# Kernel optimization log

Hardware: AMD Instinct MI355X
Metric: run time of the kernel (lower is better)

## Reference

```python
import jax, jax.numpy as jnp
import numpy as np
from functools import partial

T, B, CH, H, W = 16, 4, 128, 128, 128
TAU, VTH, ALPHA, EPS = 2.0, 1.0, 2.0, 1e-5

# ATan surrogate-gradient spike (spikingjelly surrogate.ATan, alpha=2.0)
@jax.custom_vjp
def spike(x):
    return (x >= 0.0).astype(x.dtype)

def _spike_fwd(x):
    return spike(x), x

def _spike_bwd(x, g):
    return (g * (ALPHA / 2.0) / (1.0 + (jnp.pi / 2.0 * ALPHA * x) ** 2),)

spike.defvjp(_spike_fwd, _spike_bwd)

def _conv(x, w):  # x [N,C,H,W], w [O,I,3,3], padding=1 -> SAME
    return jax.lax.conv_general_dilated(x, w, (1, 1), 'SAME',
                                        dimension_numbers=('NCHW', 'OIHW', 'NCHW'))

def _bn(x, g, b, m, v):  # inference-mode BatchNorm2d, channel axis 1
    inv = g / jnp.sqrt(v + EPS)
    return x * inv[:, None, None] + (b - m * inv)[:, None, None]

def _pool(x):  # MaxPool2d(2,2), NCHW
    return jax.lax.reduce_window(x, -jnp.inf, jax.lax.max,
                                 (1, 1, 2, 2), (1, 1, 2, 2), 'VALID')

def _lif(xs):  # xs [T, ...]; LIFNode: tau=2, v_th=1, v_reset=0, decay_input, hard reset (detached)
    def step(v, x):
        v = v + (x - v) / TAU                      # charge
        s = spike(v - VTH)                         # fire (Heaviside fwd, ATan bwd)
        v = v * (1.0 - jax.lax.stop_gradient(s))   # detached hard reset to 0
        return v, s
    return jax.lax.scan(step, jnp.zeros_like(xs[0]), xs)[1]

def _block(xs, w, g, b, m, v):  # conv -> BN -> LIF -> maxpool, xs [T,B,C,H,W]
    t, bs = xs.shape[0], xs.shape[1]
    y = _bn(_conv(xs.reshape((t * bs,) + xs.shape[2:]), w), g, b, m, v)
    y = _lif(y.reshape((t, bs) + y.shape[1:]))
    y = _pool(y.reshape((t * bs,) + y.shape[2:]))
    return y.reshape((t, bs) + y.shape[1:])


def setup_inputs() -> dict:
    key = jax.random.key(0)
    ks = jax.random.split(key, 8)
    inp = {'x': jax.random.uniform(ks[0], (T, B, 2, H, W), jnp.float32)}
    fan_ins = [2 * 9, CH * 9, CH * 9, CH * 9]
    for i in range(4):
        cin = 2 if i == 0 else CH
        inp[f'w{i+1}'] = jax.random.normal(ks[i + 1], (CH, cin, 3, 3), jnp.float32) * np.sqrt(2.0 / fan_ins[i]).astype(np.float32)
        inp[f'g{i+1}'] = jnp.ones((CH,), jnp.float32)
        inp[f'b{i+1}'] = jnp.zeros((CH,), jnp.float32)
        inp[f'm{i+1}'] = jnp.zeros((CH,), jnp.float32)
        inp[f'v{i+1}'] = jnp.ones((CH,), jnp.float32)
    inp['wfc'] = jax.random.normal(ks[5], (10, CH * 8 * 8), jnp.float32) * np.sqrt(1.0 / (CH * 64)).astype(np.float32)
    inp['bfc'] = jnp.zeros((10,), jnp.float32)
    return inp


def reference(x, w1, g1, b1, m1, v1, w2, g2, b2, m2, v2,
              w3, g3, b3, m3, v3, w4, g4, b4, m4, v4, wfc, bfc):
    y = _block(x, w1, g1, b1, m1, v1)   # [T,B,CH,64,64]
    y = _block(y, w2, g2, b2, m2, v2)   # [T,B,CH,32,32]
    y = _block(y, w3, g3, b3, m3, v3)   # [T,B,CH,16,16]
    y = _block(y, w4, g4, b4, m4, v4)   # [T,B,CH,8,8]
    z = y.reshape(y.shape[0], y.shape[1], -1) @ wfc.T + bfc  # [T,B,10]
    return _lif(z)                       # output spike train [T,B,10]
```

## Files before the change

### kernel.cpp

```cpp
#include <hip/hip_runtime.h>
#include <hip/hip_bf16.h>
#include <math.h>

#define T_STEPS 16

typedef __attribute__((ext_vector_type(8))) short bf16x8;
typedef __attribute__((ext_vector_type(16))) float f32x16;

__global__ __launch_bounds__(256) void prep_w_kernel(const float* __restrict__ w,
                                                     __hip_bfloat16* __restrict__ wp) {
  int idx = blockIdx.x * 256 + threadIdx.x;
  if (idx >= 147456) return;
  int co = idx / 1152, rem = idx - co * 1152;
  int ci = rem / 9, tap = rem - ci * 9;
  float x = w[idx];
  float h = (float)__float2bfloat16(x);
  float r1 = x - h;
  float m = (float)__float2bfloat16(r1);
  float r2 = r1 - m;
  size_t base = (((size_t)tap * 16 + (ci >> 3)) * 128 + co) * 8 + (ci & 7);
  const size_t SSZ = 147456;
  wp[base] = __float2bfloat16(h);
  wp[SSZ + base] = __float2bfloat16(m);
  wp[2 * SSZ + base] = __float2bfloat16(r2);
}

__global__ __launch_bounds__(192) void pad_x_kernel(const float* __restrict__ x,
                                                    float* __restrict__ xp) {
  const int plane = blockIdx.x;
  const int row = blockIdx.y;
  const int c = threadIdx.x;
  if (c < 132) {
    float v = 0.f;
    int gr = row - 1, gc = c - 1;
    if ((unsigned)gr < 128u && (unsigned)gc < 128u)
      v = x[(size_t)plane * 16384 + gr * 128 + gc];
    xp[((size_t)plane * 130 + row) * 132 + c] = v;
  }
}

__global__ __launch_bounds__(256) void layer1_kernel(
    const float* __restrict__ xp, const float* __restrict__ w,
    const float* __restrict__ gn, const float* __restrict__ bn,
    const float* __restrict__ mn, const float* __restrict__ vn,
    __hip_bfloat16* __restrict__ out) {
  const int tid = threadIdx.x;
  const int tile = blockIdx.x;
  const int ty0 = (tile >> 2) * 32, tx0 = (tile & 3) * 32;
  const int co0 = blockIdx.y * 4;
  const int b = blockIdx.z;
  const int qx2 = (tid & 15) * 2;
  const int qy2 = (tid >> 4) * 2;
  const int yq = ty0 + qy2;
  const int xq = tx0 + qx2;

  float wreg[2][9][4];
#pragma unroll
  for (int j = 0; j < 4; ++j)
#pragma unroll
    for (int ci = 0; ci < 2; ++ci)
#pragma unroll
      for (int tap = 0; tap < 9; ++tap)
        wreg[ci][tap][j] = w[(co0 + j) * 18 + ci * 9 + tap];

  float scale[4], shift[4];
#pragma unroll
  for (int j = 0; j < 4; ++j) {
    float inv = gn[co0 + j] / sqrtf(vn[co0 + j] + 1e-5f);
    scale[j] = inv;
    shift[j] = bn[co0 + j] - mn[co0 + j] * inv;
  }

  float vm[4][4];
#pragma unroll
  for (int j = 0; j < 4; ++j)
#pragma unroll
    for (int p = 0; p < 4; ++p) vm[j][p] = 0.f;

  for (int t = 0; t < T_STEPS; ++t) {
    const float* xpt = xp + (size_t)((t * 4 + b) * 2) * 17160;
    float iv[2][4][4];
#pragma unroll
    for (int ci = 0; ci < 2; ++ci)
#pragma unroll
      for (int r = 0; r < 4; ++r)
        *(float4*)&iv[ci][r][0] =
            *(const float4*)(xpt + (size_t)(ci * 130 + yq + r) * 132 + xq);

    float acc[4][4];
#pragma unroll
    for (int j = 0; j < 4; ++j)
#pragma unroll
      for (int p = 0; p < 4; ++p) acc[j][p] = 0.f;

#pragma unroll
    for (int ci = 0; ci < 2; ++ci)
#pragma unroll
      for (int tap = 0; tap < 9; ++tap) {
        const int dy = tap / 3, dx = tap - dy * 3;
#pragma unroll
        for (int sy = 0; sy < 2; ++sy)
#pragma unroll
          for (int sx = 0; sx < 2; ++sx) {
            float xin = iv[ci][sy + dy][sx + dx];
            acc[0][sy * 2 + sx] += wreg[ci][tap][0] * xin;
            acc[1][sy * 2 + sx] += wreg[ci][tap][1] * xin;
            acc[2][sy * 2 + sx] += wreg[ci][tap][2] * xin;
            acc[3][sy * 2 + sx] += wreg[ci][tap][3] * xin;
          }
      }

    const int py = (ty0 >> 1) + (tid >> 4);
    const int px = (tx0 >> 1) + (tid & 15);
    short4 pk;
    short* pks = (short*)&pk;
#pragma unroll
    for (int j = 0; j < 4; ++j) {
      float mx = -1e30f;
#pragma unroll
      for (int p = 0; p < 4; ++p) {
        float yv = acc[j][p] * scale[j] + shift[j];
        float nv = vm[j][p] + (yv - vm[j][p]) * 0.5f;
        mx = fmaxf(mx, nv);
        vm[j][p] = (nv >= 1.0f) ? 0.f : nv;
      }
      __hip_bfloat16 bv = __float2bfloat16(mx >= 1.0f ? 1.0f : 0.0f);
      pks[j] = *(short*)&bv;
    }
    *(short4*)(out + (((size_t)(t * 4 + b) * 64 + py) * 64 + px) * 128 + co0) = pk;
  }
}

template <int S>
__global__ __launch_bounds__(256) void conv32_kernel(
    const __hip_bfloat16* __restrict__ spk, const __hip_bfloat16* __restrict__ wp,
    float* __restrict__ pre, int t_base) {
  constexpr int TILES_X = S / 8;
  const int tile = blockIdx.x;
  const int ty0 = (tile / TILES_X) * 16;
  const int tx0 = (tile % TILES_X) * 8;
  const int tbl = blockIdx.z;
  const int tbg = t_base * 4 + tbl;
  const int tid = threadIdx.x;
  const int lane = tid & 63;
  const int wv = tid >> 6;

  __shared__ uint4 At4[2880];

  const __hip_bfloat16* sp = spk + (size_t)tbg * S * S * 128;
#pragma unroll
  for (int k = 0; k < 12; ++k) {
    int job = k * 256 + tid;
    if (job < 2880) {
      int c8 = job & 15, r = job >> 4;
      int y = (r * 6554) >> 16;
      int xx = r - y * 10;
      int gy = ty0 - 1 + y, gx = tx0 - 1 + xx;
      uint4 v = make_uint4(0u, 0u, 0u, 0u);
      if ((unsigned)gy < (unsigned)S && (unsigned)gx < (unsigned)S)
        v = *(const uint4*)(sp + ((size_t)(gy * S + gx)) * 128 + c8 * 8);
      At4[(y * 10 + xx) * 16 + (c8 ^ (xx & 7))] = v;
    }
  }
  __syncthreads();

  const int l31 = lane & 31, hh = lane >> 5;
  const int co = wv * 32 + l31;
  const int ly = l31 >> 3, lx = lane & 7;

  f32x16 acc[4];
#pragma unroll
  for (int m = 0; m < 4; ++m)
#pragma unroll
    for (int r = 0; r < 16; ++r) acc[m][r] = 0.f;

  const short* wpb = (const short*)wp + (size_t)co * 8;

  for (int tap = 0; tap < 9; ++tap) {
    const int dy = tap / 3, dx = tap - dy * 3;
    const int xx = lx + dx;
    const int sx7 = xx & 7;
#pragma unroll
    for (int kk = 0; kk < 8; ++kk) {
      const int kc = kk * 2 + hh;
      bf16x8 a[4];
#pragma unroll
      for (int m = 0; m < 4; ++m)
        a[m] = *(const bf16x8*)(At4 + ((m * 4 + ly + dy) * 10 + xx) * 16 + (kc ^ sx7));
#pragma unroll
      for (int s = 0; s < 3; ++s) {
        bf16x8 bfr = *(const bf16x8*)(wpb + ((size_t)(s * 9 + tap) * 16 + kc) * 1024);
#pragma unroll
        for (int m = 0; m < 4; ++m)
          acc[m] = __builtin_amdgcn_mfma_f32_32x32x16_bf16(a[m], bfr, acc[m], 0, 0, 0);
      }
    }
  }

  float* po = pre + (size_t)tbl * S * S * 128 + co;
#pragma unroll
  for (int m = 0; m < 4; ++m)
#pragma unroll
    for (int r = 0; r < 16; ++r) {
      int row = (r & 3) + 8 * (r >> 2) + 4 * hh;
      int p = m * 32 + row;
      po[((size_t)(ty0 + (p >> 3)) * S + tx0 + (p & 7)) * 128] = acc[m][r];
    }
}

template <int S>
__global__ __launch_bounds__(256) void lif_pool_kernel(
    const float* __restrict__ pre, __hip_bfloat16* __restrict__ spk,
    float* __restrict__ vm, const float* __restrict__ gn,
    const float* __restrict__ bn, const float* __restrict__ mn,
    const float* __restrict__ vn, int t_base, int nt) {
  constexpr int OS = S / 2, NQ = OS * OS;
  const int tid = threadIdx.x;
  const int co = tid & 127;
  const int q = blockIdx.x * 2 + (tid >> 7);
  const int b = blockIdx.z;
  const int qy = q / OS, qx = q - qy * OS;
  float inv = gn[co] / sqrtf(vn[co] + 1e-5f);
  float sc = inv, sh = bn[co] - mn[co] * inv;
  float* vp = vm + (((size_t)b * NQ + q) * 4) * 128 + co;
  float v0, v1, v2, v3;
  if (t_base == 0) {
    v0 = v1 = v2 = v3 = 0.f;
  } else {
    v0 = vp[0]; v1 = vp[128]; v2 = vp[256]; v3 = vp[384];
  }
  const size_t rowstride = (size_t)S * 128;
  for (int t = 0; t < nt; ++t) {
    const float* p = pre + (((size_t)(t * 4 + b) * S + qy * 2) * S + qx * 2) * 128 + co;
    float x00 = p[0] * sc + sh;
    float x01 = p[128] * sc + sh;
    float x10 = p[rowstride] * sc + sh;
    float x11 = p[rowstride + 128] * sc + sh;
    float n0 = v0 + (x00 - v0) * 0.5f; float s0 = n0 >= 1.f ? 1.f : 0.f; v0 = n0 >= 1.f ? 0.f : n0;
    float n1 = v1 + (x01 - v1) * 0.5f; float s1 = n1 >= 1.f ? 1.f : 0.f; v1 = n1 >= 1.f ? 0.f : n1;
    float n2 = v2 + (x10 - v2) * 0.5f; float s2 = n2 >= 1.f ? 1.f : 0.f; v2 = n2 >= 1.f ? 0.f : n2;
    float n3 = v3 + (x11 - v3) * 0.5f; float s3 = n3 >= 1.f ? 1.f : 0.f; v3 = n3 >= 1.f ? 0.f : n3;
    float pooled = fmaxf(fmaxf(s0, s1), fmaxf(s2, s3));
    spk[((size_t)((t_base + t) * 4 + b) * NQ + q) * 128 + co] = __float2bfloat16(pooled);
  }
  if (t_base + nt < T_STEPS) {
    vp[0] = v0; vp[128] = v1; vp[256] = v2; vp[384] = v3;
  }
}

__global__ __launch_bounds__(256) void fc_kernel(const __hip_bfloat16* __restrict__ a4,
                                                 const float* __restrict__ wfc,
                                                 const float* __restrict__ bfc,
                                                 float* __restrict__ z) {
  const int tb = blockIdx.x;
  const int tid = threadIdx.x;
  const __hip_bfloat16* a = a4 + (size_t)tb * 8192;
  float part[10];
#pragma unroll
  for (int o = 0; o < 10; ++o) part[o] = 0.f;
  for (int i = tid; i < 8192; i += 256) {
    int co = i >> 6, yx = i & 63;
    float av = __bfloat162float(a[yx * 128 + co]);
#pragma unroll
    for (int o = 0; o < 10; ++o) part[o] += av * wfc[o * 8192 + i];
  }
#pragma unroll
  for (int o = 0; o < 10; ++o)
    for (int off = 32; off > 0; off >>= 1) part[o] += __shfl_xor(part[o], off, 64);
  __shared__ float red[4][10];
  if ((tid & 63) == 0) {
#pragma unroll
    for (int o = 0; o < 10; ++o) red[tid >> 6][o] = part[o];
  }
  __syncthreads();
  if (tid < 10)
    z[tb * 10 + tid] = red[0][tid] + red[1][tid] + red[2][tid] + red[3][tid] + bfc[tid];
}

__global__ void out_lif_kernel(const float* __restrict__ z, float* __restrict__ out) {
  int i = threadIdx.x;
  if (i < 40) {
    float v = 0.f;
    for (int t = 0; t < T_STEPS; ++t) {
      float yv = z[t * 40 + i];
      float nv = v + (yv - v) * 0.5f;
      float s = (nv >= 1.0f) ? 1.0f : 0.0f;
      out[t * 40 + i] = s;
      v = (nv >= 1.0f) ? 0.f : nv;
    }
  }
}

extern "C" void kernel_launch(void* const* d_in, const int* in_sizes, int n_in,
                              void* d_out, int out_size, void* d_ws, size_t ws_size,
                              hipStream_t stream) {
  const float* x = (const float*)d_in[0];
  const float* w1 = (const float*)d_in[1];
  const float* g1 = (const float*)d_in[2];
  const float* b1 = (const float*)d_in[3];
  const float* m1 = (const float*)d_in[4];
  const float* v1 = (const float*)d_in[5];
  const float* w2 = (const float*)d_in[6];
  const float* g2 = (const float*)d_in[7];
  const float* b2 = (const float*)d_in[8];
  const float* m2 = (const float*)d_in[9];
  const float* v2 = (const float*)d_in[10];
  const float* w3 = (const float*)d_in[11];
  const float* g3 = (const float*)d_in[12];
  const float* b3 = (const float*)d_in[13];
  const float* m3 = (const float*)d_in[14];
  const float* v3 = (const float*)d_in[15];
  const float* w4 = (const float*)d_in[16];
  const float* g4 = (const float*)d_in[17];
  const float* b4 = (const float*)d_in[18];
  const float* m4 = (const float*)d_in[19];
  const float* v4 = (const float*)d_in[20];
  const float* wfc = (const float*)d_in[21];
  const float* bfc = (const float*)d_in[22];
  float* out = (float*)d_out;

  float* p = (float*)d_ws;
  __hip_bfloat16* wp2 = (__hip_bfloat16*)p; p += 221184;
  __hip_bfloat16* wp3 = (__hip_bfloat16*)p; p += 221184;
  __hip_bfloat16* wp4 = (__hip_bfloat16*)p; p += 221184;
  __hip_bfloat16* spk1 = (__hip_bfloat16*)p; p += 16777216;
  float* preH = p; p += 16777216;
  float* xp = preH;
  __hip_bfloat16* spk2 = (__hip_bfloat16*)p; p += 4194304;
  float* vm2 = p; p += 2097152;
  __hip_bfloat16* spk3 = (__hip_bfloat16*)p; p += 1048576;
  float* vm3 = p; p += 524288;
  __hip_bfloat16* spk4 = (__hip_bfloat16*)p; p += 262144;
  float* vm4 = p; p += 131072;
  float* z = p; p += 640;

  prep_w_kernel<<<576, 256, 0, stream>>>(w2, wp2);
  prep_w_kernel<<<576, 256, 0, stream>>>(w3, wp3);
  prep_w_kernel<<<576, 256, 0, stream>>>(w4, wp4);
  pad_x_kernel<<<dim3(128, 130), 192, 0, stream>>>(x, xp);

  layer1_kernel<<<dim3(16, 32, 4), 256, 0, stream>>>(xp, w1, g1, b1, m1, v1, spk1);

  conv32_kernel<64><<<dim3(32, 1, 32), 256, 0, stream>>>(spk1, wp2, preH, 0);
  lif_pool_kernel<64><<<dim3(512, 1, 4), 256, 0, stream>>>(preH, spk2, vm2, g2, b2, m2, v2, 0, 8);
  conv32_kernel<64><<<dim3(32, 1, 32), 256, 0, stream>>>(spk1, wp2, preH, 8);
  lif_pool_kernel<64><<<dim3(512, 1, 4), 256, 0, stream>>>(preH, spk2, vm2, g2, b2, m2, v2, 8, 8);

  conv32_kernel<32><<<dim3(8, 1, 64), 256, 0, stream>>>(spk2, wp3, preH, 0);
  lif_pool_kernel<32><<<dim3(128, 1, 4), 256, 0, stream>>>(preH, spk3, vm3, g3, b3, m3, v3, 0, 16);

  conv32_kernel<16><<<dim3(2, 1, 64), 256, 0, stream>>>(spk3, wp4, preH, 0);
  lif_pool_kernel<16><<<dim3(32, 1, 4), 256, 0, stream>>>(preH, spk4, vm4, g4, b4, m4, v4, 0, 16);

  fc_kernel<<<64, 256, 0, stream>>>(spk4, wfc, bfc, z);
  out_lif_kernel<<<1, 64, 0, stream>>>(z, out);
}
```

Measured before the change: 450.7 us.

## Process two time-batch slices per conv block to reuse weight fragments

Adds a conv kernel where each block loads input tiles for two (t,b) slices into shared memory. Each weight fragment is then reused across 8 MFMAs instead of 4, halving weight loads per unit of work. Layer 2 now runs in four smaller chunks with a half-size pre-activation buffer, which may improve L2 residency. It also merges the three weight-prep launches into one. In exchange, each block uses twice the LDS and accumulator registers, and the grid is halved, both of which lower occupancy.

```diff
diff --git a/kernel.cpp b/kernel.cpp
--- a/kernel.cpp
+++ b/kernel.cpp
@@ -7,8 +7,12 @@
 typedef __attribute__((ext_vector_type(8))) short bf16x8;
 typedef __attribute__((ext_vector_type(16))) float f32x16;
 
-__global__ __launch_bounds__(256) void prep_w_kernel(const float* __restrict__ w,
-                                                     __hip_bfloat16* __restrict__ wp) {
+__global__ __launch_bounds__(256) void prep_w3_kernel(
+    const float* __restrict__ w2, const float* __restrict__ w3,
+    const float* __restrict__ w4, __hip_bfloat16* __restrict__ wp2,
+    __hip_bfloat16* __restrict__ wp3, __hip_bfloat16* __restrict__ wp4) {
+  const float* w = blockIdx.y == 0 ? w2 : (blockIdx.y == 1 ? w3 : w4);
+  __hip_bfloat16* wp = blockIdx.y == 0 ? wp2 : (blockIdx.y == 1 ? wp3 : wp4);
   int idx = blockIdx.x * 256 + threadIdx.x;
   if (idx >= 147456) return;
   int co = idx / 1152, rem = idx - co * 1152;
@@ -129,6 +133,94 @@
     }
     *(short4*)(out + (((size_t)(t * 4 + b) * 64 + py) * 64 + px) * 128 + co0) = pk;
   }
+}
+
+template <int S>
+__global__ __launch_bounds__(256) void conv32_tb2_kernel(
+    const __hip_bfloat16* __restrict__ spk, const __hip_bfloat16* __restrict__ wp,
+    float* __restrict__ pre, int tb_base) {
+  constexpr int TILES_X = S / 8;
+  const int tile = blockIdx.x;
+  const int ty0 = (tile / TILES_X) * 16;
+  const int tx0 = (tile % TILES_X) * 8;
+  const int pair = blockIdx.z;
+  const int tbl0 = pair * 2;
+  const int tb0 = tb_base + tbl0;
+  const int tid = threadIdx.x;
+  const int lane = tid & 63;
+  const int wv = tid >> 6;
+
+  __shared__ uint4 At4[2][2880];
+
+#pragma unroll
+  for (int i = 0; i < 2; ++i) {
+    const __hip_bfloat16* sp = spk + (size_t)(tb0 + i) * S * S * 128;
+    for (int job = tid; job < 2880; job += 256) {
+      int c8 = job & 15, r = job >> 4;
+      int y = (r * 6554) >> 16;
+      int xx = r - y * 10;
+      int gy = ty0 - 1 + y, gx = tx0 - 1 + xx;
+      uint4 v = make_uint4(0u, 0u, 0u, 0u);
+      if ((unsigned)gy < (unsigned)S && (unsigned)gx < (unsigned)S)
+        v = *(const uint4*)(sp + ((size_t)(gy * S + gx)) * 128 + c8 * 8);
+      At4[i][(y * 10 + xx) * 16 + (c8 ^ (xx & 7))] = v;
+    }
+  }
+  __syncthreads();
+
+  const int l31 = lane & 31, hh = lane >> 5;
+  const int co = wv * 32 + l31;
+  const int ly = l31 >> 3, lx = lane & 7;
+  const uint4* A0 = &At4[0][0];
+  const uint4* A1 = &At4[1][0];
+
+  f32x16 acc0[4], acc1[4];
+#pragma unroll
+  for (int m = 0; m < 4; ++m)
+#pragma unroll
+    for (int r = 0; r < 16; ++r) { acc0[m][r] = 0.f; acc1[m][r] = 0.f; }
+
+  const short* wpb = (const short*)wp + (size_t)co * 8;
+
+  for (int tap = 0; tap < 9; ++tap) {
+    const int dy = tap / 3, dx = tap - dy * 3;
+    const int xx = lx + dx;
+    const int sx7 = xx & 7;
+#pragma unroll
+    for (int kk = 0; kk < 8; ++kk) {
+      const int kc = kk * 2 + hh;
+      bf16x8 a0[4], a1[4];
+#pragma unroll
+      for (int m = 0; m < 4; ++m) {
+        const int slot = ((m * 4 + ly + dy) * 10 + xx) * 16 + (kc ^ sx7);
+        a0[m] = *(const bf16x8*)(A0 + slot);
+        a1[m] = *(const bf16x8*)(A1 + slot);
+      }
+#pragma unroll
+      for (int s = 0; s < 3; ++s) {
+        bf16x8 bfr = *(const bf16x8*)(wpb + ((size_t)(s * 9 + tap) * 16 + kc) * 1024);
+#pragma unroll
+        for (int m = 0; m < 4; ++m)
+          acc0[m] = __builtin_amdgcn_mfma_f32_32x32x16_bf16(a0[m], bfr, acc0[m], 0, 0, 0);
+#pragma unroll
+        for (int m = 0; m < 4; ++m)
+          acc1[m] = __builtin_amdgcn_mfma_f32_32x32x16_bf16(a1[m], bfr, acc1[m], 0, 0, 0);
+      }
+    }
+  }
+
+  float* po0 = pre + (size_t)tbl0 * S * S * 128 + co;
+  float* po1 = pre + (size_t)(tbl0 + 1) * S * S * 128 + co;
+#pragma unroll
+  for (int m = 0; m < 4; ++m)
+#pragma unroll
+    for (int r = 0; r < 16; ++r) {
+      int row = (r & 3) + 8 * (r >> 2) + 4 * hh;
+      int p = m * 32 + row;
+      size_t off = ((size_t)(ty0 + (p >> 3)) * S + tx0 + (p & 7)) * 128;
+      po0[off] = acc0[m][r];
+      po1[off] = acc1[m][r];
+    }
 }
 
 template <int S>
@@ -324,7 +416,7 @@
   __hip_bfloat16* wp3 = (__hip_bfloat16*)p; p += 221184;
   __hip_bfloat16* wp4 = (__hip_bfloat16*)p; p += 221184;
   __hip_bfloat16* spk1 = (__hip_bfloat16*)p; p += 16777216;
-  float* preH = p; p += 16777216;
+  float* preH = p; p += 8388608;
   float* xp = preH;
   __hip_bfloat16* spk2 = (__hip_bfloat16*)p; p += 4194304;
   float* vm2 = p; p += 2097152;
@@ -334,19 +426,18 @@
   float* vm4 = p; p += 131072;
   float* z = p; p += 640;
 
-  prep_w_kernel<<<576, 256, 0, stream>>>(w2, wp2);
-  prep_w_kernel<<<576, 256, 0, stream>>>(w3, wp3);
-  prep_w_kernel<<<576, 256, 0, stream>>>(w4, wp4);
+  prep_w3_kernel<<<dim3(576, 3), 256, 0, stream>>>(w2, w3, w4, wp2, wp3, wp4);
   pad_x_kernel<<<dim3(128, 130), 192, 0, stream>>>(x, xp);
 
   layer1_kernel<<<dim3(16, 32, 4), 256, 0, stream>>>(xp, w1, g1, b1, m1, v1, spk1);
 
-  conv32_kernel<64><<<dim3(32, 1, 32), 256, 0, stream>>>(spk1, wp2, preH, 0);
-  lif_pool_kernel<64><<<dim3(512, 1, 4), 256, 0, stream>>>(preH, spk2, vm2, g2, b2, m2, v2, 0, 8);
-  conv32_kernel<64><<<dim3(32, 1, 32), 256, 0, stream>>>(spk1, wp2, preH, 8);
-  lif_pool_kernel<64><<<dim3(512, 1, 4), 256, 0, stream>>>(preH, spk2, vm2, g2, b2, m2, v2, 8, 8);
-
-  conv32_kernel<32><<<dim3(8, 1, 64), 256, 0, stream>>>(spk2, wp3, preH, 0);
+  for (int c = 0; c < 4; ++c) {
+    conv32_tb2_kernel<64><<<dim3(32, 1, 8), 256, 0, stream>>>(spk1, wp2, preH, c * 16);
+    lif_pool_kernel<64><<<dim3(512, 1, 4), 256, 0, stream>>>(preH, spk2, vm2, g2, b2,
+                                                             m2, v2, c * 4, 4);
+  }
+
+  conv32_tb2_kernel<32><<<dim3(8, 1, 32), 256, 0, stream>>>(spk2, wp3, preH, 0);
   lif_pool_kernel<32><<<dim3(128, 1, 4), 256, 0, stream>>>(preH, spk3, vm3, g3, b3, m3, v3, 0, 16);
 
   conv32_kernel<16><<<dim3(2, 1, 64), 256, 0, stream>>>(spk3, wp4, preH, 0);
```

Result: slower. 519.7 us (+15.3%).
